# Optimization experiments

Hardware: AMD Instinct MI355X
Metric: run time of the kernel (lower is better)

Reference implementation:

```python
import jax, jax.numpy as jnp
import numpy as np

B, P1, P, N = 4, 12, 12, 207
D_MODEL, D_K, H, D_HID = 128, 16, 8, 256
LN_EPS = 1e-5


def setup_inputs() -> dict:
    key = jax.random.key(0)
    ks = jax.random.split(key, 11)
    s = 1.0 / np.sqrt(D_MODEL)
    return {
        "inputs": jax.random.normal(ks[0], (B, P1, N, D_MODEL), jnp.float32),
        "enc_K": jax.random.normal(ks[1], (B, P, N, H, D_K), jnp.float32),
        "enc_V": jax.random.normal(ks[2], (B, P, N, H, D_K), jnp.float32),
        "c_targets": jax.random.normal(ks[3], (B, P1, N, D_MODEL), jnp.float32),
        # MetaLearner params
        "W1": jax.random.normal(ks[4], (D_HID, D_MODEL), jnp.float32) * s,
        "b1": jnp.zeros((D_HID,), jnp.float32),
        "W2": jax.random.normal(ks[5], (H * D_K * D_MODEL, D_HID), jnp.float32) * (1.0 / np.sqrt(D_HID)),
        "b2": jnp.zeros((H * D_K * D_MODEL,), jnp.float32),
        # output projection (no bias) + layernorm
        "W_out": jax.random.normal(ks[6], (D_MODEL, D_MODEL), jnp.float32) * s,
        "gamma": jnp.ones((D_MODEL,), jnp.float32),
        "beta": jnp.zeros((D_MODEL,), jnp.float32),
    }


def reference(inputs, enc_K, enc_V, c_targets, W1, b1, W2, b2, W_out, gamma, beta):
    # --- MetaLearner: hypernetwork producing per-token Q weights ---
    h = jax.nn.relu(jnp.einsum("bpnd,hd->bpnh", c_targets, W1) + b1)  # (B,P1,N,D_HID)
    w = jnp.einsum("bpnh,oh->bpno", h, W2) + b2                        # (B,P1,N,H*dk*dm)
    W_q = w.reshape(B, P1, N, H, D_K, D_MODEL)

    # --- per-token batched matvec: Q = W_q @ inputs ---
    Q = jnp.einsum("bqnhkd,bqnd->bqnhk", W_q, inputs)                  # (B,P1,N,H,dk)

    # --- multi-head temporal attention over the P axis (non-causal) ---
    scores = jnp.einsum("bqnhk,bpnhk->bnhqp", Q, enc_K) / np.sqrt(D_K)
    alpha = jax.nn.softmax(scores, axis=-1)                            # (B,N,H,P1,P)
    out = jnp.einsum("bnhqp,bpnhk->bqnhk", alpha, enc_V)
    out = out.reshape(B, P1, N, H * D_K)                               # (B,P1,N,d_model)

    # --- output projection + residual + layernorm ---
    out = jnp.einsum("bqnd,od->bqno", out, W_out) + inputs
    mu = jnp.mean(out, axis=-1, keepdims=True)
    var = jnp.var(out, axis=-1, keepdims=True)
    out = (out - mu) * jax.lax.rsqrt(var + LN_EPS) * gamma + beta
    return out
```

## Files before the change

### kernel.cpp

```cpp
#include <hip/hip_runtime.h>
#include <hip/hip_bf16.h>

#define NB    4
#define NP    12
#define NN_   207
#define DM    128
#define DHID  256
#define M_TOK 9936
#define M_PAD 9984
#define KSPLIT 8

typedef float        f32x4 __attribute__((ext_vector_type(4)));
typedef unsigned int u32x4 __attribute__((ext_vector_type(4)));
typedef __bf16       bf16x8 __attribute__((ext_vector_type(8)));

static __device__ __forceinline__ unsigned int pk_bf2(float a, float b) {
    __hip_bfloat16 ba = __float2bfloat16(a);
    __hip_bfloat16 bb = __float2bfloat16(b);
    unsigned short ua = *reinterpret_cast<unsigned short*>(&ba);
    unsigned short ub = *reinterpret_cast<unsigned short*>(&bb);
    return (unsigned int)ua | ((unsigned int)ub << 16);
}
static __device__ __forceinline__ unsigned int cvt_pk_bf16(float lo, float hi) {
    unsigned int r;
    asm("v_cvt_pk_bf16_f32 %0, %1, %2" : "=v"(r) : "v"(lo), "v"(hi));
    return r;
}

__global__ __launch_bounds__(256) void k_prep(const float* __restrict__ W2,
                                              unsigned short* __restrict__ W2b,
                                              const float* __restrict__ x,
                                              float* __restrict__ xT,
                                              const float* __restrict__ ct,
                                              const float* __restrict__ W1,
                                              const float* __restrict__ b1,
                                              const float* __restrict__ b2,
                                              float* __restrict__ hb,
                                              float* __restrict__ Qb) {
    const int t = threadIdx.x;
    const int bid = blockIdx.x;
    if (bid < 2048) {
        int i = bid * 256 + t;
        const f32x4* in = reinterpret_cast<const f32x4*>(W2);
        f32x4 v0 = in[2 * i], v1 = in[2 * i + 1];
        u32x4 o;
        o[0] = pk_bf2(v0[0], v0[1]);
        o[1] = pk_bf2(v0[2], v0[3]);
        o[2] = pk_bf2(v1[0], v1[1]);
        o[3] = pk_bf2(v1[2], v1[3]);
        reinterpret_cast<u32x4*>(W2b)[i] = o;
        return;
    }
    if (bid < 3296) {
        __shared__ float tile[32][33];
        const int b = bid - 2048;
        const int bm = b >> 2;
        const int bd = b & 3;
        const int m0 = bm * 32, d0 = bd * 32;
        #pragma unroll
        for (int i = 0; i < 4; ++i) {
            int e = i * 256 + t;
            int lm = e >> 5, ld = e & 31;
            int m = m0 + lm;
            tile[lm][ld] = (m < M_TOK) ? x[(size_t)m * DM + d0 + ld] : 0.0f;
        }
        __syncthreads();
        #pragma unroll
        for (int i = 0; i < 4; ++i) {
            int e = i * 256 + t;
            int ld = e >> 5, lm = e & 31;
            xT[(size_t)(d0 + ld) * M_PAD + m0 + lm] = tile[lm][ld];
        }
        return;
    }
    __shared__ unsigned short AB[128 * 128];
    __shared__ unsigned short WB[64 * 128];
    const int m0 = (bid - 3296) * 128;
    const int w = t >> 6, l = t & 63;
    const int lr = l & 15, g = l >> 4;

    #pragma unroll
    for (int it = 0; it < 8; ++it) {
        int r = (t >> 4) + it * 16;
        int gg = t & 15;
        int m = m0 + r;
        f32x4 a = (f32x4)(0.0f), b = (f32x4)(0.0f);
        if (m < M_TOK) {
            a = *reinterpret_cast<const f32x4*>(&ct[(size_t)m * DM + gg * 8]);
            b = *reinterpret_cast<const f32x4*>(&ct[(size_t)m * DM + gg * 8 + 4]);
        }
        u32x4 pk;
        pk[0] = pk_bf2(a[0], a[1]); pk[1] = pk_bf2(a[2], a[3]);
        pk[2] = pk_bf2(b[0], b[1]); pk[3] = pk_bf2(b[2], b[3]);
        *reinterpret_cast<u32x4*>(&AB[r * 128 + ((gg ^ (r & 7)) * 8)]) = pk;
    }

    for (int jc = 0; jc < 4; ++jc) {
        __syncthreads();
        #pragma unroll
        for (int it = 0; it < 4; ++it) {
            int r = (t >> 4) + it * 16;
            int gg = t & 15;
            const float* src = &W1[(size_t)(jc * 64 + r) * DM + gg * 8];
            f32x4 a = *reinterpret_cast<const f32x4*>(src);
            f32x4 b = *reinterpret_cast<const f32x4*>(src + 4);
            u32x4 pk;
            pk[0] = pk_bf2(a[0], a[1]); pk[1] = pk_bf2(a[2], a[3]);
            pk[2] = pk_bf2(b[0], b[1]); pk[3] = pk_bf2(b[2], b[3]);
            *reinterpret_cast<u32x4*>(&WB[r * 128 + ((gg ^ (r & 7)) * 8)]) = pk;
        }
        __syncthreads();
        f32x4 acc[2][4];
        #pragma unroll
        for (int a2 = 0; a2 < 2; ++a2)
            #pragma unroll
            for (int jf = 0; jf < 4; ++jf) acc[a2][jf] = (f32x4)(0.0f);
        #pragma unroll
        for (int ks = 0; ks < 4; ++ks) {
            bf16x8 A2[2], B4[4];
            #pragma unroll
            for (int tf = 0; tf < 2; ++tf) {
                int row = (2 * w + tf) * 16 + lr;
                A2[tf] = *reinterpret_cast<const bf16x8*>(
                    &AB[row * 128 + (((ks * 4 + g) ^ (row & 7)) * 8)]);
            }
            #pragma unroll
            for (int jf = 0; jf < 4; ++jf) {
                int row = jf * 16 + lr;
                B4[jf] = *reinterpret_cast<const bf16x8*>(
                    &WB[row * 128 + (((ks * 4 + g) ^ (row & 7)) * 8)]);
            }
            #pragma unroll
            for (int tf = 0; tf < 2; ++tf)
                #pragma unroll
                for (int jf = 0; jf < 4; ++jf)
                    acc[tf][jf] = __builtin_amdgcn_mfma_f32_16x16x32_bf16(
                        A2[tf], B4[jf], acc[tf][jf], 0, 0, 0);
        }
        #pragma unroll
        for (int jf = 0; jf < 4; ++jf) {
            int j = jc * 64 + jf * 16 + lr;
            float bv = b1[j];
            #pragma unroll
            for (int tf = 0; tf < 2; ++tf)
                #pragma unroll
                for (int rr = 0; rr < 4; ++rr) {
                    int m = m0 + (2 * w + tf) * 16 + g * 4 + rr;
                    if (m < M_TOK)
                        hb[(size_t)m * DHID + j] = fmaxf(acc[tf][jf][rr] + bv, 0.0f);
                }
        }
    }

    __syncthreads();
    #pragma unroll
    for (int it = 0; it < 8; ++it) {
        int r = (t >> 4) + it * 16;
        int gg = t & 15;
        int m = m0 + r;
        f32x4 a = (f32x4)(0.0f), b = (f32x4)(0.0f);
        if (m < M_TOK) {
            a = *reinterpret_cast<const f32x4*>(&x[(size_t)m * DM + gg * 8]);
            b = *reinterpret_cast<const f32x4*>(&x[(size_t)m * DM + gg * 8 + 4]);
        }
        u32x4 pk;
        pk[0] = pk_bf2(a[0], a[1]); pk[1] = pk_bf2(a[2], a[3]);
        pk[2] = pk_bf2(b[0], b[1]); pk[3] = pk_bf2(b[2], b[3]);
        *reinterpret_cast<u32x4*>(&AB[r * 128 + ((gg ^ (r & 7)) * 8)]) = pk;
    }
    for (int oc = 0; oc < 2; ++oc) {
        #pragma unroll
        for (int it = 0; it < 4; ++it) {
            int r = (t >> 4) + it * 16;
            int gg = t & 15;
            const float* src = &b2[(size_t)(oc * 64 + r) * DM + gg * 8];
            f32x4 a = *reinterpret_cast<const f32x4*>(src);
            f32x4 b = *reinterpret_cast<const f32x4*>(src + 4);
            u32x4 pk;
            pk[0] = pk_bf2(a[0], a[1]); pk[1] = pk_bf2(a[2], a[3]);
            pk[2] = pk_bf2(b[0], b[1]); pk[3] = pk_bf2(b[2], b[3]);
            *reinterpret_cast<u32x4*>(&WB[r * 128 + ((gg ^ (r & 7)) * 8)]) = pk;
        }
        __syncthreads();
        f32x4 acc[2][4];
        #pragma unroll
        for (int a2 = 0; a2 < 2; ++a2)
            #pragma unroll
            for (int of = 0; of < 4; ++of) acc[a2][of] = (f32x4)(0.0f);
        #pragma unroll
        for (int ks = 0; ks < 4; ++ks) {
            bf16x8 A2[2], B4[4];
            #pragma unroll
            for (int tf = 0; tf < 2; ++tf) {
                int row = (2 * w + tf) * 16 + lr;
                A2[tf] = *reinterpret_cast<const bf16x8*>(
                    &AB[row * 128 + (((ks * 4 + g) ^ (row & 7)) * 8)]);
            }
            #pragma unroll
            for (int of = 0; of < 4; ++of) {
                int row = of * 16 + lr;
                B4[of] = *reinterpret_cast<const bf16x8*>(
                    &WB[row * 128 + (((ks * 4 + g) ^ (row & 7)) * 8)]);
            }
            #pragma unroll
            for (int tf = 0; tf < 2; ++tf)
                #pragma unroll
                for (int of = 0; of < 4; ++of)
                    acc[tf][of] = __builtin_amdgcn_mfma_f32_16x16x32_bf16(
                        A2[tf], B4[of], acc[tf][of], 0, 0, 0);
        }
        #pragma unroll
        for (int of = 0; of < 4; ++of) {
            int o = oc * 64 + of * 16 + lr;
            #pragma unroll
            for (int tf = 0; tf < 2; ++tf)
                #pragma unroll
                for (int rr = 0; rr < 4; ++rr) {
                    int m = m0 + (2 * w + tf) * 16 + g * 4 + rr;
                    if (m < M_TOK) Qb[(size_t)m * DM + o] = acc[tf][of][rr];
                }
        }
        __syncthreads();
    }
}

__global__ __launch_bounds__(256, 2) void k_gemm(const unsigned short* __restrict__ W2b,
                                                 const float* __restrict__ hbuf,
                                                 const float* __restrict__ xT,
                                                 float* __restrict__ Qp) {
    __shared__ unsigned short As[2][160 * 32];
    __shared__ unsigned short Bs[2][128 * 32];
    const int t = threadIdx.x;
    const int kid = blockIdx.x & 7;
    const int mb  = blockIdx.x >> 3;
    const int m0 = mb * 160;
    const int j0 = kid * 32;
    const int w = t >> 6, l = t & 63;
    const int wo  = w & 1;
    const int wmi = w >> 1;
    const int lr = l & 15, g = l >> 4;

    const int rA = t >> 2;
    const int c  = t & 3;
    const bool has3 = (t < 128);
    const int aw = rA * 32 + ((c ^ ((rA >> 1) & 3)) * 8);

    const float* h1p = &hbuf[(size_t)(m0 + rA) * DHID + j0 + c * 8];
    const float* h2p = &hbuf[(size_t)(m0 + 64 + rA) * DHID + j0 + c * 8];
    const f32x4 h1a = *reinterpret_cast<const f32x4*>(h1p);
    const f32x4 h1b = *reinterpret_cast<const f32x4*>(h1p + 4);
    const f32x4 h2a = *reinterpret_cast<const f32x4*>(h2p);
    const f32x4 h2b = *reinterpret_cast<const f32x4*>(h2p + 4);
    f32x4 h3a = (f32x4)(0.0f), h3b = (f32x4)(0.0f);
    if (has3) {
        const float* h3p = &hbuf[(size_t)(m0 + 128 + rA) * DHID + j0 + c * 8];
        h3a = *reinterpret_cast<const f32x4*>(h3p);
        h3b = *reinterpret_cast<const f32x4*>(h3p + 4);
    }

    f32x4 acc[5][4];
    #pragma unroll
    for (int fo = 0; fo < 5; ++fo)
        #pragma unroll
        for (int ot = 0; ot < 4; ++ot) acc[fo][ot] = (f32x4)(0.0f);

    const unsigned short* bp1 = W2b + (size_t)rA * 32768 + j0 + c * 8;
    const unsigned short* bp2 = bp1 + (size_t)64 * 32768;
    const float* xp = xT + m0 + rA;

    const int rswz = (g ^ ((lr >> 1) & 3)) * 8;
    const int aBase = wmi * 2560 + lr * 32 + rswz;
    const int bBase = wo * 2048 + lr * 32 + rswz;

#define STAGE(BUF, BV1, BV2, XV1, XV2, XV3) do {                       \
        u32x4 a_;                                                      \
        a_[0] = cvt_pk_bf16((XV1) * h1a[0], (XV1) * h1a[1]);           \
        a_[1] = cvt_pk_bf16((XV1) * h1a[2], (XV1) * h1a[3]);           \
        a_[2] = cvt_pk_bf16((XV1) * h1b[0], (XV1) * h1b[1]);           \
        a_[3] = cvt_pk_bf16((XV1) * h1b[2], (XV1) * h1b[3]);           \
        *reinterpret_cast<u32x4*>(&As[BUF][aw]) = a_;                  \
        a_[0] = cvt_pk_bf16((XV2) * h2a[0], (XV2) * h2a[1]);           \
        a_[1] = cvt_pk_bf16((XV2) * h2a[2], (XV2) * h2a[3]);           \
        a_[2] = cvt_pk_bf16((XV2) * h2b[0], (XV2) * h2b[1]);           \
        a_[3] = cvt_pk_bf16((XV2) * h2b[2], (XV2) * h2b[3]);           \
        *reinterpret_cast<u32x4*>(&As[BUF][aw + 2048]) = a_;           \
        if (has3) {                                                    \
            a_[0] = cvt_pk_bf16((XV3) * h3a[0], (XV3) * h3a[1]);       \
            a_[1] = cvt_pk_bf16((XV3) * h3a[2], (XV3) * h3a[3]);       \
            a_[2] = cvt_pk_bf16((XV3) * h3b[0], (XV3) * h3b[1]);       \
            a_[3] = cvt_pk_bf16((XV3) * h3b[2], (XV3) * h3b[3]);       \
            *reinterpret_cast<u32x4*>(&As[BUF][aw + 4096]) = a_;       \
        }                                                              \
        *reinterpret_cast<u32x4*>(&Bs[BUF][aw]) = (BV1);               \
        *reinterpret_cast<u32x4*>(&Bs[BUF][aw + 2048]) = (BV2);        \
    } while (0)

    {
        u32x4 bv1 = *reinterpret_cast<const u32x4*>(bp1);
        u32x4 bv2 = *reinterpret_cast<const u32x4*>(bp2);
        float x1 = xp[0], x2 = xp[64], x3 = xp[128];
        STAGE(0, bv1, bv2, x1, x2, x3);
    }
    u32x4 nb1 = *reinterpret_cast<const u32x4*>(bp1 + 256);
    u32x4 nb2 = *reinterpret_cast<const u32x4*>(bp2 + 256);
    float nx1 = xp[M_PAD], nx2 = xp[M_PAD + 64], nx3 = xp[M_PAD + 128];
    __syncthreads();

    int cur = 0;
    for (int d = 0; d < 128; ++d) {
        u32x4 bfr0 = *reinterpret_cast<const u32x4*>(&Bs[cur][bBase]);
        u32x4 bfr1 = *reinterpret_cast<const u32x4*>(&Bs[cur][bBase + 512]);
        u32x4 bfr2 = *reinterpret_cast<const u32x4*>(&Bs[cur][bBase + 1024]);
        u32x4 bfr3 = *reinterpret_cast<const u32x4*>(&Bs[cur][bBase + 1536]);
        if (d < 127) STAGE(cur ^ 1, nb1, nb2, nx1, nx2, nx3);
        if (d < 126) {
            nb1 = *reinterpret_cast<const u32x4*>(bp1 + (size_t)(d + 2) * 256);
            nb2 = *reinterpret_cast<const u32x4*>(bp2 + (size_t)(d + 2) * 256);
            const float* xq = xp + (size_t)(d + 2) * M_PAD;
            nx1 = xq[0]; nx2 = xq[64]; nx3 = xq[128];
        }
        __builtin_amdgcn_s_setprio(1);
        #pragma unroll
        for (int fo = 0; fo < 5; ++fo) {
            u32x4 afr = *reinterpret_cast<const u32x4*>(&As[cur][aBase + fo * 512]);
            asm("v_mfma_f32_16x16x32_bf16 %0, %1, %2, %0" : "+v"(acc[fo][0]) : "v"(afr), "v"(bfr0));
            asm("v_mfma_f32_16x16x32_bf16 %0, %1, %2, %0" : "+v"(acc[fo][1]) : "v"(afr), "v"(bfr1));
            asm("v_mfma_f32_16x16x32_bf16 %0, %1, %2, %0" : "+v"(acc[fo][2]) : "v"(afr), "v"(bfr2));
            asm("v_mfma_f32_16x16x32_bf16 %0, %1, %2, %0" : "+v"(acc[fo][3]) : "v"(afr), "v"(bfr3));
        }
        __builtin_amdgcn_s_setprio(0);
        __syncthreads();
        cur ^= 1;
    }
#undef STAGE

    float* outp = Qp + (size_t)kid * M_PAD * DM;
    #pragma unroll
    for (int fo = 0; fo < 5; ++fo)
        #pragma unroll
        for (int ot = 0; ot < 4; ++ot)
            #pragma unroll
            for (int rr = 0; rr < 4; ++rr) {
                int m = m0 + wmi * 80 + fo * 16 + g * 4 + rr;
                int o = wo * 64 + ot * 16 + lr;
                if (m < M_TOK) outp[(size_t)m * DM + o] = acc[fo][ot][rr];
            }
}

__global__ __launch_bounds__(256) void k_attn(const float* __restrict__ Qp,
                                              const float* __restrict__ Qb,
                                              const float* __restrict__ Kenc,
                                              const float* __restrict__ Venc,
                                              const float* __restrict__ xin,
                                              const float* __restrict__ Wout,
                                              const float* __restrict__ gamma,
                                              const float* __restrict__ beta,
                                              float* __restrict__ out) {
    __shared__ float Qs[12][132];
    __shared__ float Ks[12][132];
    __shared__ float Vs[12][132];
    __shared__ float Ss[12][12][8];
    __shared__ float Os[12][132];
    const int t = threadIdx.x;
    const int b = blockIdx.x / NN_;
    const int n = blockIdx.x % NN_;

    for (int e = t; e < 384; e += 256) {
        int row = e >> 5, c4 = e & 31;
        size_t mrow = (size_t)(b * NP + row) * NN_ + n;
        f32x4 q = *reinterpret_cast<const f32x4*>(&Qb[mrow * DM + c4 * 4]);
        #pragma unroll
        for (int k = 0; k < KSPLIT; ++k)
            q += *reinterpret_cast<const f32x4*>(&Qp[((size_t)k * M_PAD + mrow) * DM + c4 * 4]);
        *reinterpret_cast<f32x4*>(&Qs[row][c4 * 4]) = q;
        *reinterpret_cast<f32x4*>(&Ks[row][c4 * 4]) =
            *reinterpret_cast<const f32x4*>(&Kenc[mrow * DM + c4 * 4]);
        *reinterpret_cast<f32x4*>(&Vs[row][c4 * 4]) =
            *reinterpret_cast<const f32x4*>(&Venc[mrow * DM + c4 * 4]);
    }
    __syncthreads();
    if (t < 144) {
        int q = t / 12, p = t % 12;
        #pragma unroll
        for (int hh = 0; hh < 8; ++hh) {
            const f32x4* qv = reinterpret_cast<const f32x4*>(&Qs[q][hh * 16]);
            const f32x4* kv = reinterpret_cast<const f32x4*>(&Ks[p][hh * 16]);
            float s = 0.0f;
            #pragma unroll
            for (int c = 0; c < 4; ++c) {
                f32x4 a = qv[c], bb = kv[c];
                s += a[0] * bb[0] + a[1] * bb[1] + a[2] * bb[2] + a[3] * bb[3];
            }
            Ss[q][p][hh] = s * 0.25f;
        }
    }
    __syncthreads();
    if (t < 96) {
        int q = t >> 3, hh = t & 7;
        float mx = -1e30f;
        #pragma unroll
        for (int p = 0; p < 12; ++p) mx = fmaxf(mx, Ss[q][p][hh]);
        float ev[12]; float sum = 0.0f;
        #pragma unroll
        for (int p = 0; p < 12; ++p) { ev[p] = __expf(Ss[q][p][hh] - mx); sum += ev[p]; }
        float inv = 1.0f / sum;
        #pragma unroll
        for (int p = 0; p < 12; ++p) Ss[q][p][hh] = ev[p] * inv;
    }
    __syncthreads();
    #pragma unroll
    for (int i = 0; i < 6; ++i) {
        int e = i * 256 + t;
        int q = e >> 7, hk = e & 127, hh = hk >> 4;
        float acc = 0.0f;
        #pragma unroll
        for (int p = 0; p < 12; ++p) acc += Ss[q][p][hh] * Vs[p][hk];
        Os[q][hk] = acc;
    }
    __syncthreads();
    {
        const int o  = t & 127;
        const int qh = (t >> 7) * 6;
        const f32x4* wrow = reinterpret_cast<const f32x4*>(&Wout[(size_t)o * DM]);
        float pacc[6] = {0, 0, 0, 0, 0, 0};
        for (int c = 0; c < 32; ++c) {
            f32x4 wv = wrow[c];
            #pragma unroll
            for (int qq = 0; qq < 6; ++qq) {
                f32x4 ov = *reinterpret_cast<const f32x4*>(&Os[qh + qq][c * 4]);
                pacc[qq] += wv[0] * ov[0] + wv[1] * ov[1] + wv[2] * ov[2] + wv[3] * ov[3];
            }
        }
        #pragma unroll
        for (int qq = 0; qq < 6; ++qq) {
            size_t mrow = (size_t)(b * NP + qh + qq) * NN_ + n;
            Qs[qh + qq][o] = pacc[qq] + xin[mrow * DM + o];
        }
    }
    __syncthreads();
    const int wv_ = t >> 6, ll = t & 63;
    for (int rq = wv_; rq < 12; rq += 4) {
        float v0 = Qs[rq][ll], v1 = Qs[rq][ll + 64];
        float s = v0 + v1, ss = v0 * v0 + v1 * v1;
        #pragma unroll
        for (int msk = 1; msk < 64; msk <<= 1) {
            s += __shfl_xor(s, msk, 64);
            ss += __shfl_xor(ss, msk, 64);
        }
        float mu = s * (1.0f / 128.0f);
        float var = ss * (1.0f / 128.0f) - mu * mu;
        float rs = rsqrtf(var + 1e-5f);
        size_t mrow = (size_t)(b * NP + rq) * NN_ + n;
        out[mrow * DM + ll]      = (v0 - mu) * rs * gamma[ll] + beta[ll];
        out[mrow * DM + ll + 64] = (v1 - mu) * rs * gamma[ll + 64] + beta[ll + 64];
    }
}

extern "C" void kernel_launch(void* const* d_in, const int* in_sizes, int n_in,
                              void* d_out, int out_size, void* d_ws, size_t ws_size,
                              hipStream_t stream) {
    const float* xin   = (const float*)d_in[0];
    const float* Kenc  = (const float*)d_in[1];
    const float* Venc  = (const float*)d_in[2];
    const float* ct    = (const float*)d_in[3];
    const float* W1    = (const float*)d_in[4];
    const float* b1    = (const float*)d_in[5];
    const float* W2    = (const float*)d_in[6];
    const float* b2    = (const float*)d_in[7];
    const float* Wout  = (const float*)d_in[8];
    const float* gamma = (const float*)d_in[9];
    const float* beta  = (const float*)d_in[10];
    float* out = (float*)d_out;

    char* ws = (char*)d_ws;
    unsigned short* W2b = (unsigned short*)(ws);
    float* xT  = (float*)(ws + 8388608);
    float* hb  = (float*)(ws + 13500416);
    float* Qb  = (float*)(ws + 23724032);
    float* Qp  = (float*)(ws + 28835840);

    hipLaunchKernelGGL(k_prep, dim3(3374), dim3(256), 0, stream,
                       W2, W2b, xin, xT, ct, W1, b1, b2, hb, Qb);
    hipLaunchKernelGGL(k_gemm, dim3(504), dim3(256), 0, stream, W2b, hb, xT, Qp);
    hipLaunchKernelGGL(k_attn, dim3(828), dim3(256), 0, stream, Qp, Qb, Kenc, Venc,
                       xin, Wout, gamma, beta, out);
}
```

Before: 150.6 us.

## Process two d-slices per pipeline stage in hypernetwork GEMM to halve barriers

The k_gemm main loop now stages two consecutive d-slices of A and B into shared memory per iteration and runs 64 iterations instead of 128. This halves the number of __syncthreads barriers and gives more MFMA work between them. It doubles LDS use per block and increases register pressure from the extra prefetched B fragments and x values. That could lower occupancy under launch_bounds(256,2).

```diff
diff --git a/kernel.cpp b/kernel.cpp
--- a/kernel.cpp
+++ b/kernel.cpp
@@ -228,8 +228,8 @@
                                                  const float* __restrict__ hbuf,
                                                  const float* __restrict__ xT,
                                                  float* __restrict__ Qp) {
-    __shared__ unsigned short As[2][160 * 32];
-    __shared__ unsigned short Bs[2][128 * 32];
+    __shared__ unsigned short As[2][10240];
+    __shared__ unsigned short Bs[2][8192];
     const int t = threadIdx.x;
     const int kid = blockIdx.x & 7;
     const int mb  = blockIdx.x >> 3;
@@ -272,61 +272,88 @@
     const int aBase = wmi * 2560 + lr * 32 + rswz;
     const int bBase = wo * 2048 + lr * 32 + rswz;
 
-#define STAGE(BUF, BV1, BV2, XV1, XV2, XV3) do {                       \
+#define STAGE(BUF, SA, SB, BV1, BV2, XV1, XV2, XV3) do {               \
         u32x4 a_;                                                      \
         a_[0] = cvt_pk_bf16((XV1) * h1a[0], (XV1) * h1a[1]);           \
         a_[1] = cvt_pk_bf16((XV1) * h1a[2], (XV1) * h1a[3]);           \
         a_[2] = cvt_pk_bf16((XV1) * h1b[0], (XV1) * h1b[1]);           \
         a_[3] = cvt_pk_bf16((XV1) * h1b[2], (XV1) * h1b[3]);           \
-        *reinterpret_cast<u32x4*>(&As[BUF][aw]) = a_;                  \
+        *reinterpret_cast<u32x4*>(&As[BUF][(SA) + aw]) = a_;           \
         a_[0] = cvt_pk_bf16((XV2) * h2a[0], (XV2) * h2a[1]);           \
         a_[1] = cvt_pk_bf16((XV2) * h2a[2], (XV2) * h2a[3]);           \
         a_[2] = cvt_pk_bf16((XV2) * h2b[0], (XV2) * h2b[1]);           \
         a_[3] = cvt_pk_bf16((XV2) * h2b[2], (XV2) * h2b[3]);           \
-        *reinterpret_cast<u32x4*>(&As[BUF][aw + 2048]) = a_;           \
+        *reinterpret_cast<u32x4*>(&As[BUF][(SA) + aw + 2048]) = a_;    \
         if (has3) {                                                    \
             a_[0] = cvt_pk_bf16((XV3) * h3a[0], (XV3) * h3a[1]);       \
             a_[1] = cvt_pk_bf16((XV3) * h3a[2], (XV3) * h3a[3]);       \
             a_[2] = cvt_pk_bf16((XV3) * h3b[0], (XV3) * h3b[1]);       \
             a_[3] = cvt_pk_bf16((XV3) * h3b[2], (XV3) * h3b[3]);       \
-            *reinterpret_cast<u32x4*>(&As[BUF][aw + 4096]) = a_;       \
+            *reinterpret_cast<u32x4*>(&As[BUF][(SA) + aw + 4096]) = a_; \
         }                                                              \
-        *reinterpret_cast<u32x4*>(&Bs[BUF][aw]) = (BV1);               \
-        *reinterpret_cast<u32x4*>(&Bs[BUF][aw + 2048]) = (BV2);        \
+        *reinterpret_cast<u32x4*>(&Bs[BUF][(SB) + aw]) = (BV1);        \
+        *reinterpret_cast<u32x4*>(&Bs[BUF][(SB) + aw + 2048]) = (BV2); \
     } while (0)
 
     {
         u32x4 bv1 = *reinterpret_cast<const u32x4*>(bp1);
         u32x4 bv2 = *reinterpret_cast<const u32x4*>(bp2);
-        float x1 = xp[0], x2 = xp[64], x3 = xp[128];
-        STAGE(0, bv1, bv2, x1, x2, x3);
-    }
-    u32x4 nb1 = *reinterpret_cast<const u32x4*>(bp1 + 256);
-    u32x4 nb2 = *reinterpret_cast<const u32x4*>(bp2 + 256);
-    float nx1 = xp[M_PAD], nx2 = xp[M_PAD + 64], nx3 = xp[M_PAD + 128];
+        STAGE(0, 0, 0, bv1, bv2, xp[0], xp[64], xp[128]);
+        bv1 = *reinterpret_cast<const u32x4*>(bp1 + 256);
+        bv2 = *reinterpret_cast<const u32x4*>(bp2 + 256);
+        STAGE(0, 5120, 4096, bv1, bv2, xp[M_PAD], xp[M_PAD + 64], xp[M_PAD + 128]);
+    }
+    u32x4 nb1a = *reinterpret_cast<const u32x4*>(bp1 + 512);
+    u32x4 nb2a = *reinterpret_cast<const u32x4*>(bp2 + 512);
+    u32x4 nb1b = *reinterpret_cast<const u32x4*>(bp1 + 768);
+    u32x4 nb2b = *reinterpret_cast<const u32x4*>(bp2 + 768);
+    const float* xq2 = xp + 2 * (size_t)M_PAD;
+    const float* xq3 = xp + 3 * (size_t)M_PAD;
+    float nx1a = xq2[0], nx2a = xq2[64], nx3a = xq2[128];
+    float nx1b = xq3[0], nx2b = xq3[64], nx3b = xq3[128];
     __syncthreads();
 
     int cur = 0;
-    for (int d = 0; d < 128; ++d) {
-        u32x4 bfr0 = *reinterpret_cast<const u32x4*>(&Bs[cur][bBase]);
-        u32x4 bfr1 = *reinterpret_cast<const u32x4*>(&Bs[cur][bBase + 512]);
-        u32x4 bfr2 = *reinterpret_cast<const u32x4*>(&Bs[cur][bBase + 1024]);
-        u32x4 bfr3 = *reinterpret_cast<const u32x4*>(&Bs[cur][bBase + 1536]);
-        if (d < 127) STAGE(cur ^ 1, nb1, nb2, nx1, nx2, nx3);
-        if (d < 126) {
-            nb1 = *reinterpret_cast<const u32x4*>(bp1 + (size_t)(d + 2) * 256);
-            nb2 = *reinterpret_cast<const u32x4*>(bp2 + (size_t)(d + 2) * 256);
-            const float* xq = xp + (size_t)(d + 2) * M_PAD;
-            nx1 = xq[0]; nx2 = xq[64]; nx3 = xq[128];
+    for (int wd = 0; wd < 64; ++wd) {
+        u32x4 bfA0 = *reinterpret_cast<const u32x4*>(&Bs[cur][bBase]);
+        u32x4 bfA1 = *reinterpret_cast<const u32x4*>(&Bs[cur][bBase + 512]);
+        u32x4 bfA2 = *reinterpret_cast<const u32x4*>(&Bs[cur][bBase + 1024]);
+        u32x4 bfA3 = *reinterpret_cast<const u32x4*>(&Bs[cur][bBase + 1536]);
+        u32x4 bfB0 = *reinterpret_cast<const u32x4*>(&Bs[cur][bBase + 4096]);
+        u32x4 bfB1 = *reinterpret_cast<const u32x4*>(&Bs[cur][bBase + 4608]);
+        u32x4 bfB2 = *reinterpret_cast<const u32x4*>(&Bs[cur][bBase + 5120]);
+        u32x4 bfB3 = *reinterpret_cast<const u32x4*>(&Bs[cur][bBase + 5632]);
+        if (wd < 63) {
+            STAGE(cur ^ 1, 0, 0, nb1a, nb2a, nx1a, nx2a, nx3a);
+            STAGE(cur ^ 1, 5120, 4096, nb1b, nb2b, nx1b, nx2b, nx3b);
+        }
+        if (wd < 62) {
+            const int d4 = 2 * wd + 4, d5 = 2 * wd + 5;
+            nb1a = *reinterpret_cast<const u32x4*>(bp1 + (size_t)d4 * 256);
+            nb2a = *reinterpret_cast<const u32x4*>(bp2 + (size_t)d4 * 256);
+            nb1b = *reinterpret_cast<const u32x4*>(bp1 + (size_t)d5 * 256);
+            nb2b = *reinterpret_cast<const u32x4*>(bp2 + (size_t)d5 * 256);
+            const float* xq4 = xp + (size_t)d4 * M_PAD;
+            const float* xq5 = xp + (size_t)d5 * M_PAD;
+            nx1a = xq4[0]; nx2a = xq4[64]; nx3a = xq4[128];
+            nx1b = xq5[0]; nx2b = xq5[64]; nx3b = xq5[128];
         }
         __builtin_amdgcn_s_setprio(1);
         #pragma unroll
         for (int fo = 0; fo < 5; ++fo) {
             u32x4 afr = *reinterpret_cast<const u32x4*>(&As[cur][aBase + fo * 512]);
-            asm("v_mfma_f32_16x16x32_bf16 %0, %1, %2, %0" : "+v"(acc[fo][0]) : "v"(afr), "v"(bfr0));
-            asm("v_mfma_f32_16x16x32_bf16 %0, %1, %2, %0" : "+v"(acc[fo][1]) : "v"(afr), "v"(bfr1));
-            asm("v_mfma_f32_16x16x32_bf16 %0, %1, %2, %0" : "+v"(acc[fo][2]) : "v"(afr), "v"(bfr2));
-            asm("v_mfma_f32_16x16x32_bf16 %0, %1, %2, %0" : "+v"(acc[fo][3]) : "v"(afr), "v"(bfr3));
+            asm("v_mfma_f32_16x16x32_bf16 %0, %1, %2, %0" : "+v"(acc[fo][0]) : "v"(afr), "v"(bfA0));
+            asm("v_mfma_f32_16x16x32_bf16 %0, %1, %2, %0" : "+v"(acc[fo][1]) : "v"(afr), "v"(bfA1));
+            asm("v_mfma_f32_16x16x32_bf16 %0, %1, %2, %0" : "+v"(acc[fo][2]) : "v"(afr), "v"(bfA2));
+            asm("v_mfma_f32_16x16x32_bf16 %0, %1, %2, %0" : "+v"(acc[fo][3]) : "v"(afr), "v"(bfA3));
+        }
+        #pragma unroll
+        for (int fo = 0; fo < 5; ++fo) {
+            u32x4 afr = *reinterpret_cast<const u32x4*>(&As[cur][aBase + 5120 + fo * 512]);
+            asm("v_mfma_f32_16x16x32_bf16 %0, %1, %2, %0" : "+v"(acc[fo][0]) : "v"(afr), "v"(bfB0));
+            asm("v_mfma_f32_16x16x32_bf16 %0, %1, %2, %0" : "+v"(acc[fo][1]) : "v"(afr), "v"(bfB1));
+            asm("v_mfma_f32_16x16x32_bf16 %0, %1, %2, %0" : "+v"(acc[fo][2]) : "v"(afr), "v"(bfB2));
+            asm("v_mfma_f32_16x16x32_bf16 %0, %1, %2, %0" : "+v"(acc[fo][3]) : "v"(afr), "v"(bfB3));
         }
         __builtin_amdgcn_s_setprio(0);
         __syncthreads();
```

Result: no change. 149.9 us (-0.5%).
